# Kernel tuning notes

Measured on AMD Instinct MI355X. Metric: run time of the kernel, lower is better.

## Reference

```python
import jax, jax.numpy as jnp
import numpy as np

D_IN = 1024
D_OUT = 1024

def setup_inputs() -> dict:
    key = jax.random.key(0)
    kx, kq, kk, kv = jax.random.split(key, 4)
    x = jax.random.normal(kx, (4, 4096, D_IN), dtype=jnp.float32)
    s = 1.0 / np.sqrt(D_IN)
    Wq = jax.random.uniform(kq, (D_IN, D_OUT), dtype=jnp.float32, minval=-s, maxval=s)
    Wk = jax.random.uniform(kk, (D_IN, D_OUT), dtype=jnp.float32, minval=-s, maxval=s)
    Wv = jax.random.uniform(kv, (D_IN, D_OUT), dtype=jnp.float32, minval=-s, maxval=s)
    return {"x": x, "Wq": Wq, "Wk": Wk, "Wv": Wv}

def reference(x, Wq, Wk, Wv):
    # x: [B, S, d_in]; single-head causal attention (dropout p=0 => identity)
    B, S, _ = x.shape
    Q = jnp.einsum('bsd,de->bse', x, Wq)
    K = jnp.einsum('bsd,de->bse', x, Wk)
    V = jnp.einsum('bsd,de->bse', x, Wv)
    scale = 1.0 / jnp.sqrt(jnp.asarray(K.shape[-1], dtype=Q.dtype))
    scores = jnp.einsum('bqe,bke->bqk', Q, K) * scale  # [B, S, S]
    causal = jnp.tril(jnp.ones((S, S), dtype=bool))     # mask upper triangle (diag=1)
    scores = jnp.where(causal, scores, -jnp.inf)
    weights = jax.nn.softmax(scores, axis=-1)
    return jnp.einsum('bqk,bke->bqe', weights, V)
```

## Files before the change

### kernel.cpp

```cpp
#include <hip/hip_runtime.h>
#include <hip/hip_bf16.h>
#include <stdint.h>

typedef short short8 __attribute__((ext_vector_type(8)));
typedef short short4v __attribute__((ext_vector_type(4)));
typedef float f32x4 __attribute__((ext_vector_type(4)));

static __device__ __forceinline__ short f2bf(float f) {
  union { float f; uint32_t u; } v; v.f = f;
  uint32_t r = (v.u + 0x7fffu + ((v.u >> 16) & 1u)) >> 16;
  return (short)(uint16_t)r;
}
static __device__ __forceinline__ float bf2f(short h) {
  union { uint32_t u; float f; } v; v.u = ((uint32_t)(uint16_t)h) << 16;
  return v.f;
}

#define MFMA(a, b, c) __builtin_amdgcn_mfma_f32_16x16x32_bf16((a), (b), (c), 0, 0, 0)

static __device__ __forceinline__ void gload16(const short* g, short* l) {
  __builtin_amdgcn_global_load_lds(
      (const __attribute__((address_space(1))) void*)g,
      (__attribute__((address_space(3))) void*)l, 16, 0, 0);
}

static __device__ __forceinline__ void gemm_tile(
    const short* __restrict__ Ag, int lda,
    const short* __restrict__ Bg, int ldb, int kext,
    short* Alds, short* Blds, int w, int lane, f32x4 (&acc)[4][4])
{
  const int wr = (w >> 1) * 64, wc = (w & 1) * 64;
  const int lr = lane & 15, lk = lane >> 4;

  const int c0 = w * 128 + lane;
  const int c1 = c0 + 64;
  const int r0 = c0 >> 2, ch0 = (c0 & 3) ^ ((r0 >> 1) & 3);
  const int r1 = c1 >> 2, ch1 = (c1 & 3) ^ ((r1 >> 1) & 3);
  const short* a0 = Ag + (size_t)r0 * lda + ch0 * 8;
  const short* a1 = Ag + (size_t)r1 * lda + ch1 * 8;
  const short* b0 = Bg + (size_t)r0 * ldb + ch0 * 8;
  const short* b1 = Bg + (size_t)r1 * ldb + ch1 * 8;
  short* la0 = Alds + w * 1024;
  short* la1 = la0 + 512;
  short* lb0 = Blds + w * 1024;
  short* lb1 = lb0 + 512;

  int ra[4], rb[4];
#pragma unroll
  for (int mt = 0; mt < 4; ++mt) {
    int rl = wr + mt * 16 + lr;
    ra[mt] = rl * 32 + (lk ^ ((rl >> 1) & 3)) * 8;
  }
#pragma unroll
  for (int nt = 0; nt < 4; ++nt) {
    int rl = wc + nt * 16 + lr;
    rb[nt] = rl * 32 + (lk ^ ((rl >> 1) & 3)) * 8;
  }

  for (int kk = 0; kk < kext; kk += 32) {
    if (kk) __syncthreads();
    gload16(a0 + kk, la0);
    gload16(a1 + kk, la1);
    gload16(b0 + kk, lb0);
    gload16(b1 + kk, lb1);
    __syncthreads();
    short8 af[4], bfr[4];
#pragma unroll
    for (int mt = 0; mt < 4; ++mt) af[mt] = *(const short8*)&Alds[ra[mt]];
#pragma unroll
    for (int nt = 0; nt < 4; ++nt) bfr[nt] = *(const short8*)&Blds[rb[nt]];
#pragma unroll
    for (int mt = 0; mt < 4; ++mt)
#pragma unroll
      for (int nt = 0; nt < 4; ++nt)
        acc[mt][nt] = MFMA(af[mt], bfr[nt], acc[mt][nt]);
  }
}

__global__ __launch_bounds__(256)
void cvt_x(const float* __restrict__ x, short* __restrict__ xb) {
  size_t i = (size_t)blockIdx.x * 256 + threadIdx.x;
  f32x4 a = *(const f32x4*)(x + i * 8);
  f32x4 b = *(const f32x4*)(x + i * 8 + 4);
  short8 h = { f2bf(a.x), f2bf(a.y), f2bf(a.z), f2bf(a.w),
               f2bf(b.x), f2bf(b.y), f2bf(b.z), f2bf(b.w) };
  *(short8*)(xb + i * 8) = h;
}

__global__ __launch_bounds__(256)
void cvt_w(const float* __restrict__ Wq, const float* __restrict__ Wk,
           const float* __restrict__ Wv, short* __restrict__ wt) {
  __shared__ short Tl[128][136];
  const int z = blockIdx.z;
  const float* W = (z == 0) ? Wq : (z == 1) ? Wk : Wv;
  const float scale = (z == 0) ? 0.03125f : 1.0f;
  const int c0 = blockIdx.x * 128, r0 = blockIdx.y * 128;
  const int t = threadIdx.x;
#pragma unroll
  for (int j = 0; j < 16; ++j) {
    int id = j * 256 + t;
    int row = id >> 5, c4 = id & 31;
    f32x4 v = *(const f32x4*)(W + (size_t)(r0 + row) * 1024 + c0 + c4 * 4);
#pragma unroll
    for (int cc = 0; cc < 4; ++cc) Tl[c4 * 4 + cc][row] = f2bf(v[cc] * scale);
  }
  __syncthreads();
  short* dst = wt + (size_t)z * 1048576;
#pragma unroll
  for (int j = 0; j < 8; ++j) {
    int id = j * 256 + t;
    int col = id >> 4, r8 = id & 15;
    *(short8*)(dst + (size_t)(c0 + col) * 1024 + r0 + r8 * 8) =
        *(const short8*)&Tl[col][r8 * 8];
  }
}

__global__ __launch_bounds__(256)
void qkv_gemm(const short* __restrict__ xb, const short* __restrict__ wt,
              short* __restrict__ q, short* __restrict__ k,
              short* __restrict__ vt) {
  __shared__ short Alds[128 * 32], Blds[128 * 32];
  const int z = blockIdx.z;
  const int n0 = blockIdx.x * 128, m0 = blockIdx.y * 128;
  const int t = threadIdx.x, w = t >> 6, lane = t & 63;
  f32x4 acc[4][4] = {};
  gemm_tile(xb + (size_t)m0 * 1024, 1024,
            wt + (size_t)z * 1048576 + (size_t)n0 * 1024, 1024, 1024,
            Alds, Blds, w, lane, acc);
  const int lr = lane & 15, lk = lane >> 4;
  const int wr = (w >> 1) * 64, wc = (w & 1) * 64;
#pragma unroll
  for (int mt = 0; mt < 4; ++mt) {
#pragma unroll
    for (int nt = 0; nt < 4; ++nt) {
      int col = n0 + wc + nt * 16 + lr;
      int rbase = m0 + wr + mt * 16 + lk * 4;
      if (z == 2) {
        int b = rbase >> 12, s = rbase & 4095;
        short4v h = { f2bf(acc[mt][nt][0]), f2bf(acc[mt][nt][1]),
                      f2bf(acc[mt][nt][2]), f2bf(acc[mt][nt][3]) };
        *(short4v*)(vt + ((size_t)b * 1024 + col) * 4096 + s) = h;
      } else {
        short* dst = (z == 0) ? q : k;
#pragma unroll
        for (int i = 0; i < 4; ++i)
          dst[(size_t)(rbase + i) * 1024 + col] = f2bf(acc[mt][nt][i]);
      }
    }
  }
}

__global__ __launch_bounds__(256)
void s_gemm(const short* __restrict__ q, const short* __restrict__ k,
            short* __restrict__ P, float* __restrict__ lpart) {
  __shared__ short Alds[128 * 32], Blds[128 * 32];
  const int bid = blockIdx.x;
  const int b = bid & 3, tt = bid >> 2;
  int ti = (int)((sqrtf(8.f * tt + 1.f) - 1.f) * 0.5f);
  while ((ti + 1) * (ti + 2) / 2 <= tt) ++ti;
  while (ti * (ti + 1) / 2 > tt) --ti;
  const int tj = tt - ti * (ti + 1) / 2;
  const int t = threadIdx.x, w = t >> 6, lane = t & 63;
  f32x4 acc[4][4] = {};
  gemm_tile(q + ((size_t)(b * 4096 + ti * 128)) * 1024, 1024,
            k + ((size_t)(b * 4096 + tj * 128)) * 1024, 1024, 1024,
            Alds, Blds, w, lane, acc);
  const int lr = lane & 15, lk = lane >> 4;
  const int wr = (w >> 1) * 64, wc = (w & 1) * 64;
#pragma unroll
  for (int mt = 0; mt < 4; ++mt) {
    int rl0 = wr + mt * 16 + lk * 4;
#pragma unroll
    for (int i = 0; i < 4; ++i) {
      int rl = rl0 + i;
      size_t prow = ((size_t)(b * 4096 + ti * 128 + rl)) * 4096 + tj * 128;
      float rs = 0.f;
#pragma unroll
      for (int nt = 0; nt < 4; ++nt) {
        int cl = wc + nt * 16 + lr;
        float e = 0.f;
        if (ti != tj || cl <= rl) e = __expf(acc[mt][nt][i]);
        short pb = f2bf(e);
        P[prow + cl] = pb;
        rs += bf2f(pb);
      }
      rs += __shfl_xor(rs, 1);
      rs += __shfl_xor(rs, 2);
      rs += __shfl_xor(rs, 4);
      rs += __shfl_xor(rs, 8);
      if (lr == 0)
        lpart[((size_t)(tj * 2 + (w & 1))) * 16384 + b * 4096 + ti * 128 + rl] = rs;
    }
  }
}

__global__ __launch_bounds__(256)
void l_reduce(const float* __restrict__ lpart, float* __restrict__ lsum) {
  int idx = blockIdx.x * 256 + threadIdx.x;
  int qq = idx & 4095;
  int ti = qq >> 7;
  float s = 0.f;
  for (int tj = 0; tj <= ti; ++tj)
    s += lpart[(size_t)(tj * 2) * 16384 + idx] +
         lpart[(size_t)(tj * 2 + 1) * 16384 + idx];
  lsum[idx] = s;
}

__global__ __launch_bounds__(256)
void pv_gemm(const short* __restrict__ P, const short* __restrict__ vt,
             const float* __restrict__ lsum, float* __restrict__ out) {
  __shared__ short Alds[128 * 32], Blds[128 * 32];
  const int bid = blockIdx.x;
  const int b = bid & 3;
  const int r = bid >> 2;
  const int dt = r & 7;
  const int qt = 31 - (r >> 3);
  const int t = threadIdx.x, w = t >> 6, lane = t & 63;
  f32x4 acc[4][4] = {};
  gemm_tile(P + ((size_t)(b * 4096 + qt * 128)) * 4096, 4096,
            vt + ((size_t)(b * 1024 + dt * 128)) * 4096, 4096,
            (qt + 1) * 128, Alds, Blds, w, lane, acc);
  const int lr = lane & 15, lk = lane >> 4;
  const int wr = (w >> 1) * 64, wc = (w & 1) * 64;
#pragma unroll
  for (int mt = 0; mt < 4; ++mt) {
#pragma unroll
    for (int i = 0; i < 4; ++i) {
      int rl = wr + mt * 16 + lk * 4 + i;
      int grow = b * 4096 + qt * 128 + rl;
      float inv = 1.0f / lsum[grow];
#pragma unroll
      for (int nt = 0; nt < 4; ++nt) {
        int cl = wc + nt * 16 + lr;
        out[(size_t)grow * 1024 + dt * 128 + cl] = acc[mt][nt][i] * inv;
      }
    }
  }
}

extern "C" void kernel_launch(void* const* d_in, const int* in_sizes, int n_in,
                              void* d_out, int out_size, void* d_ws, size_t ws_size,
                              hipStream_t stream) {
  (void)in_sizes; (void)n_in; (void)out_size; (void)ws_size;
  const float* x  = (const float*)d_in[0];
  const float* Wq = (const float*)d_in[1];
  const float* Wk = (const float*)d_in[2];
  const float* Wv = (const float*)d_in[3];
  float* out = (float*)d_out;

  short* q_ws  = (short*)d_ws;
  short* k_ws  = q_ws + (size_t)16777216;
  short* vt_ws = k_ws + (size_t)16777216;
  short* P     = vt_ws + (size_t)16777216;
  short* xb    = P;
  float* lpart = (float*)(P + (size_t)67108864);
  float* lsum  = lpart + (size_t)33 * 2 * 16384;
  short* wt    = (short*)(lsum + 16384);

  cvt_x<<<dim3(8192), 256, 0, stream>>>(x, xb);
  cvt_w<<<dim3(8, 8, 3), 256, 0, stream>>>(Wq, Wk, Wv, wt);
  qkv_gemm<<<dim3(8, 128, 3), 256, 0, stream>>>(xb, wt, q_ws, k_ws, vt_ws);
  s_gemm<<<dim3(2112), 256, 0, stream>>>(q_ws, k_ws, P, lpart);
  l_reduce<<<dim3(64), 256, 0, stream>>>(lpart, lsum);
  pv_gemm<<<dim3(1024), 256, 0, stream>>>(P, vt_ws, lsum, out);
}
```

Before: 375.6 us.

## Replace GEMM tile loop with 4-stage LDS-pipelined 512-thread kernel

Rewrites the shared GEMM helper as a multi-buffered pipeline. Four 64-wide K stages sit in 128 KB of dynamic LDS, loads are issued three steps ahead, and completion is gated with explicit vmcnt waits and one barrier per step. Blocks grow to 512 threads with 8 waves, each computing a 64x32 sub-tile, and the partial row-sum layout widens to 4 slices per tile. The aim is to hide global-load latency and halve the barrier count per K step. In exchange it uses much more LDS, which may cap occupancy, and it depends on exact waitcnt accounting.

```diff
diff --git a/kernel.cpp b/kernel.cpp
--- a/kernel.cpp
+++ b/kernel.cpp
@@ -24,56 +24,86 @@
       (__attribute__((address_space(3))) void*)l, 16, 0, 0);
 }
 
-static __device__ __forceinline__ void gemm_tile(
+static __device__ __forceinline__ void stage_tile(
+    const short* __restrict__ Ag, int lda,
+    const short* __restrict__ Bg, int ldb, int kk,
+    short* slot, int t, int w)
+{
+#pragma unroll
+  for (int j = 0; j < 2; ++j) {
+    int idx = j * 512 + t;
+    int row = idx >> 3;
+    int cg = (idx & 7) ^ (row & 7);
+    gload16(Ag + (size_t)row * lda + kk + cg * 8, slot + j * 4096 + w * 512);
+  }
+#pragma unroll
+  for (int j = 0; j < 2; ++j) {
+    int idx = j * 512 + t;
+    int row = idx >> 3;
+    int cg = (idx & 7) ^ (row & 7);
+    gload16(Bg + (size_t)row * ldb + kk + cg * 8, slot + 8192 + j * 4096 + w * 512);
+  }
+}
+
+static __device__ __forceinline__ void gemm_pipe(
     const short* __restrict__ Ag, int lda,
     const short* __restrict__ Bg, int ldb, int kext,
-    short* Alds, short* Blds, int w, int lane, f32x4 (&acc)[4][4])
+    short* lds, int t, f32x4 (&acc)[4][2])
 {
-  const int wr = (w >> 1) * 64, wc = (w & 1) * 64;
+  const int w  = t >> 6, lane = t & 63;
   const int lr = lane & 15, lk = lane >> 4;
-
-  const int c0 = w * 128 + lane;
-  const int c1 = c0 + 64;
-  const int r0 = c0 >> 2, ch0 = (c0 & 3) ^ ((r0 >> 1) & 3);
-  const int r1 = c1 >> 2, ch1 = (c1 & 3) ^ ((r1 >> 1) & 3);
-  const short* a0 = Ag + (size_t)r0 * lda + ch0 * 8;
-  const short* a1 = Ag + (size_t)r1 * lda + ch1 * 8;
-  const short* b0 = Bg + (size_t)r0 * ldb + ch0 * 8;
-  const short* b1 = Bg + (size_t)r1 * ldb + ch1 * 8;
-  short* la0 = Alds + w * 1024;
-  short* la1 = la0 + 512;
-  short* lb0 = Blds + w * 1024;
-  short* lb1 = lb0 + 512;
-
-  int ra[4], rb[4];
-#pragma unroll
-  for (int mt = 0; mt < 4; ++mt) {
-    int rl = wr + mt * 16 + lr;
-    ra[mt] = rl * 32 + (lk ^ ((rl >> 1) & 3)) * 8;
-  }
-#pragma unroll
-  for (int nt = 0; nt < 4; ++nt) {
-    int rl = wc + nt * 16 + lr;
-    rb[nt] = rl * 32 + (lk ^ ((rl >> 1) & 3)) * 8;
-  }
-
-  for (int kk = 0; kk < kext; kk += 32) {
-    if (kk) __syncthreads();
-    gload16(a0 + kk, la0);
-    gload16(a1 + kk, la1);
-    gload16(b0 + kk, lb0);
-    gload16(b1 + kk, lb1);
-    __syncthreads();
-    short8 af[4], bfr[4];
-#pragma unroll
-    for (int mt = 0; mt < 4; ++mt) af[mt] = *(const short8*)&Alds[ra[mt]];
-#pragma unroll
-    for (int nt = 0; nt < 4; ++nt) bfr[nt] = *(const short8*)&Blds[rb[nt]];
-#pragma unroll
-    for (int mt = 0; mt < 4; ++mt)
-#pragma unroll
-      for (int nt = 0; nt < 4; ++nt)
-        acc[mt][nt] = MFMA(af[mt], bfr[nt], acc[mt][nt]);
+  const int wr64 = (w >> 2) * 64, wc32 = (w & 3) * 32;
+  const int nk = kext >> 6;
+
+  const int npro = nk < 3 ? nk : 3;
+  for (int p = 0; p < npro; ++p)
+    stage_tile(Ag, lda, Bg, ldb, p * 64, lds + p * 16384, t, w);
+
+  for (int tt = 0; tt < nk; ++tt) {
+    const int rem = nk - 1 - tt;
+    if (rem >= 2)      { asm volatile("s_waitcnt vmcnt(8)" ::: "memory"); }
+    else if (rem == 1) { asm volatile("s_waitcnt vmcnt(4)" ::: "memory"); }
+    else               { asm volatile("s_waitcnt vmcnt(0)" ::: "memory"); }
+    __builtin_amdgcn_sched_barrier(0);
+    __builtin_amdgcn_s_barrier();
+    __builtin_amdgcn_sched_barrier(0);
+
+    if (tt + 3 < nk)
+      stage_tile(Ag, lda, Bg, ldb, (tt + 3) * 64,
+                 lds + ((tt + 3) & 3) * 16384, t, w);
+
+    short* slot = lds + (tt & 3) * 16384;
+    short8 af[4][2], bfr[2][2];
+#pragma unroll
+    for (int mt = 0; mt < 4; ++mt) {
+      int rl = wr64 + mt * 16 + lr;
+#pragma unroll
+      for (int kh = 0; kh < 2; ++kh) {
+        int ch = (kh * 4 + lk) ^ (rl & 7);
+        af[mt][kh] = *(const short8*)&slot[rl * 64 + ch * 8];
+      }
+    }
+#pragma unroll
+    for (int nt = 0; nt < 2; ++nt) {
+      int rl = wc32 + nt * 16 + lr;
+#pragma unroll
+      for (int kh = 0; kh < 2; ++kh) {
+        int ch = (kh * 4 + lk) ^ (rl & 7);
+        bfr[nt][kh] = *(const short8*)&slot[8192 + rl * 64 + ch * 8];
+      }
+    }
+    __builtin_amdgcn_s_setprio(1);
+#pragma unroll
+    for (int kh = 0; kh < 2; ++kh)
+#pragma unroll
+      for (int mt = 0; mt < 4; ++mt)
+#pragma unroll
+        for (int nt = 0; nt < 2; ++nt)
+          acc[mt][nt] = MFMA(af[mt][kh], bfr[nt][kh], acc[mt][nt]);
+    __builtin_amdgcn_s_setprio(0);
+
+    asm volatile("s_waitcnt lgkmcnt(0)" ::: "memory");
+    __builtin_amdgcn_sched_barrier(0);
   }
 }
 
@@ -115,26 +145,27 @@
   }
 }
 
-__global__ __launch_bounds__(256)
+__global__ __launch_bounds__(512, 2)
 void qkv_gemm(const short* __restrict__ xb, const short* __restrict__ wt,
               short* __restrict__ q, short* __restrict__ k,
               short* __restrict__ vt) {
-  __shared__ short Alds[128 * 32], Blds[128 * 32];
+  extern __shared__ short lds[];
   const int z = blockIdx.z;
   const int n0 = blockIdx.x * 128, m0 = blockIdx.y * 128;
-  const int t = threadIdx.x, w = t >> 6, lane = t & 63;
-  f32x4 acc[4][4] = {};
-  gemm_tile(xb + (size_t)m0 * 1024, 1024,
+  const int t = threadIdx.x;
+  f32x4 acc[4][2] = {};
+  gemm_pipe(xb + (size_t)m0 * 1024, 1024,
             wt + (size_t)z * 1048576 + (size_t)n0 * 1024, 1024, 1024,
-            Alds, Blds, w, lane, acc);
+            lds, t, acc);
+  const int w = t >> 6, lane = t & 63;
   const int lr = lane & 15, lk = lane >> 4;
-  const int wr = (w >> 1) * 64, wc = (w & 1) * 64;
+  const int wr64 = (w >> 2) * 64, wc32 = (w & 3) * 32;
 #pragma unroll
   for (int mt = 0; mt < 4; ++mt) {
 #pragma unroll
-    for (int nt = 0; nt < 4; ++nt) {
-      int col = n0 + wc + nt * 16 + lr;
-      int rbase = m0 + wr + mt * 16 + lk * 4;
+    for (int nt = 0; nt < 2; ++nt) {
+      int col = n0 + wc32 + nt * 16 + lr;
+      int rbase = m0 + wr64 + mt * 16 + lk * 4;
       if (z == 2) {
         int b = rbase >> 12, s = rbase & 4095;
         short4v h = { f2bf(acc[mt][nt][0]), f2bf(acc[mt][nt][1]),
@@ -150,34 +181,35 @@
   }
 }
 
-__global__ __launch_bounds__(256)
+__global__ __launch_bounds__(512, 2)
 void s_gemm(const short* __restrict__ q, const short* __restrict__ k,
             short* __restrict__ P, float* __restrict__ lpart) {
-  __shared__ short Alds[128 * 32], Blds[128 * 32];
+  extern __shared__ short lds[];
   const int bid = blockIdx.x;
   const int b = bid & 3, tt = bid >> 2;
   int ti = (int)((sqrtf(8.f * tt + 1.f) - 1.f) * 0.5f);
   while ((ti + 1) * (ti + 2) / 2 <= tt) ++ti;
   while (ti * (ti + 1) / 2 > tt) --ti;
   const int tj = tt - ti * (ti + 1) / 2;
-  const int t = threadIdx.x, w = t >> 6, lane = t & 63;
-  f32x4 acc[4][4] = {};
-  gemm_tile(q + ((size_t)(b * 4096 + ti * 128)) * 1024, 1024,
+  const int t = threadIdx.x;
+  f32x4 acc[4][2] = {};
+  gemm_pipe(q + ((size_t)(b * 4096 + ti * 128)) * 1024, 1024,
             k + ((size_t)(b * 4096 + tj * 128)) * 1024, 1024, 1024,
-            Alds, Blds, w, lane, acc);
+            lds, t, acc);
+  const int w = t >> 6, lane = t & 63;
   const int lr = lane & 15, lk = lane >> 4;
-  const int wr = (w >> 1) * 64, wc = (w & 1) * 64;
+  const int wr64 = (w >> 2) * 64, wc32 = (w & 3) * 32;
 #pragma unroll
   for (int mt = 0; mt < 4; ++mt) {
-    int rl0 = wr + mt * 16 + lk * 4;
+    int rl0 = wr64 + mt * 16 + lk * 4;
 #pragma unroll
     for (int i = 0; i < 4; ++i) {
       int rl = rl0 + i;
       size_t prow = ((size_t)(b * 4096 + ti * 128 + rl)) * 4096 + tj * 128;
       float rs = 0.f;
 #pragma unroll
-      for (int nt = 0; nt < 4; ++nt) {
-        int cl = wc + nt * 16 + lr;
+      for (int nt = 0; nt < 2; ++nt) {
+        int cl = wc32 + nt * 16 + lr;
         float e = 0.f;
         if (ti != tj || cl <= rl) e = __expf(acc[mt][nt][i]);
         short pb = f2bf(e);
@@ -189,7 +221,7 @@
       rs += __shfl_xor(rs, 4);
       rs += __shfl_xor(rs, 8);
       if (lr == 0)
-        lpart[((size_t)(tj * 2 + (w & 1))) * 16384 + b * 4096 + ti * 128 + rl] = rs;
+        lpart[((size_t)(tj * 4 + (w & 3))) * 16384 + b * 4096 + ti * 128 + rl] = rs;
     }
   }
 }
@@ -200,38 +232,42 @@
   int qq = idx & 4095;
   int ti = qq >> 7;
   float s = 0.f;
-  for (int tj = 0; tj <= ti; ++tj)
-    s += lpart[(size_t)(tj * 2) * 16384 + idx] +
-         lpart[(size_t)(tj * 2 + 1) * 16384 + idx];
+  for (int tj = 0; tj <= ti; ++tj) {
+    s += lpart[(size_t)(tj * 4 + 0) * 16384 + idx] +
+         lpart[(size_t)(tj * 4 + 1) * 16384 + idx] +
+         lpart[(size_t)(tj * 4 + 2) * 16384 + idx] +
+         lpart[(size_t)(tj * 4 + 3) * 16384 + idx];
+  }
   lsum[idx] = s;
 }
 
-__global__ __launch_bounds__(256)
+__global__ __launch_bounds__(512, 2)
 void pv_gemm(const short* __restrict__ P, const short* __restrict__ vt,
              const float* __restrict__ lsum, float* __restrict__ out) {
-  __shared__ short Alds[128 * 32], Blds[128 * 32];
+  extern __shared__ short lds[];
   const int bid = blockIdx.x;
   const int b = bid & 3;
   const int r = bid >> 2;
   const int dt = r & 7;
   const int qt = 31 - (r >> 3);
-  const int t = threadIdx.x, w = t >> 6, lane = t & 63;
-  f32x4 acc[4][4] = {};
-  gemm_tile(P + ((size_t)(b * 4096 + qt * 128)) * 4096, 4096,
+  const int t = threadIdx.x;
+  f32x4 acc[4][2] = {};
+  gemm_pipe(P + ((size_t)(b * 4096 + qt * 128)) * 4096, 4096,
             vt + ((size_t)(b * 1024 + dt * 128)) * 4096, 4096,
-            (qt + 1) * 128, Alds, Blds, w, lane, acc);
+            (qt + 1) * 128, lds, t, acc);
+  const int w = t >> 6, lane = t & 63;
   const int lr = lane & 15, lk = lane >> 4;
-  const int wr = (w >> 1) * 64, wc = (w & 1) * 64;
+  const int wr64 = (w >> 2) * 64, wc32 = (w & 3) * 32;
 #pragma unroll
   for (int mt = 0; mt < 4; ++mt) {
 #pragma unroll
     for (int i = 0; i < 4; ++i) {
-      int rl = wr + mt * 16 + lk * 4 + i;
+      int rl = wr64 + mt * 16 + lk * 4 + i;
       int grow = b * 4096 + qt * 128 + rl;
       float inv = 1.0f / lsum[grow];
 #pragma unroll
-      for (int nt = 0; nt < 4; ++nt) {
-        int cl = wc + nt * 16 + lr;
+      for (int nt = 0; nt < 2; ++nt) {
+        int cl = wc32 + nt * 16 + lr;
         out[(size_t)grow * 1024 + dt * 128 + cl] = acc[mt][nt][i] * inv;
       }
     }
@@ -254,13 +290,21 @@
   short* P     = vt_ws + (size_t)16777216;
   short* xb    = P;
   float* lpart = (float*)(P + (size_t)67108864);
-  float* lsum  = lpart + (size_t)33 * 2 * 16384;
+  float* lsum  = lpart + (size_t)128 * 16384;
   short* wt    = (short*)(lsum + 16384);
+
+  const int gemm_lds = 4 * 16384 * 2;
+  hipFuncSetAttribute((const void*)qkv_gemm,
+                      hipFuncAttributeMaxDynamicSharedMemorySize, gemm_lds);
+  hipFuncSetAttribute((const void*)s_gemm,
+                      hipFuncAttributeMaxDynamicSharedMemorySize, gemm_lds);
+  hipFuncSetAttribute((const void*)pv_gemm,
+                      hipFuncAttributeMaxDynamicSharedMemorySize, gemm_lds);
 
   cvt_x<<<dim3(8192), 256, 0, stream>>>(x, xb);
   cvt_w<<<dim3(8, 8, 3), 256, 0, stream>>>(Wq, Wk, Wv, wt);
-  qkv_gemm<<<dim3(8, 128, 3), 256, 0, stream>>>(xb, wt, q_ws, k_ws, vt_ws);
-  s_gemm<<<dim3(2112), 256, 0, stream>>>(q_ws, k_ws, P, lpart);
+  qkv_gemm<<<dim3(8, 128, 3), 512, gemm_lds, stream>>>(xb, wt, q_ws, k_ws, vt_ws);
+  s_gemm<<<dim3(2112), 512, gemm_lds, stream>>>(q_ws, k_ws, P, lpart);
   l_reduce<<<dim3(64), 256, 0, stream>>>(lpart, lsum);
-  pv_gemm<<<dim3(1024), 256, 0, stream>>>(P, vt_ws, lsum, out);
-}
+  pv_gemm<<<dim3(1024), 512, gemm_lds, stream>>>(P, vt_ws, lsum, out);
+}
```

Result: slower. 393.7 us (+4.8%).

## Use 256x256 double-buffered pipelined GEMM tiles for QKV and score kernels

Applied to the files above, without the earlier changes.

Adds a new GEMM core that computes 256x256 output tiles with 512 threads. It uses a K-step of 64, double-buffered LDS (128KB dynamic) with XOR swizzle, and interleaves global-to-LDS prefetch of the next stage with MFMA on the current one, raising MFMA priority with setprio. The QKV projection and the causal score kernel switch to this core, and the triangular tile indexing, row-sum partials and l_reduce are adjusted for the 256 tile size. The aim is more data reuse per loaded byte and hiding of load latency. In exchange it costs more registers and LDS per block, and diagonal tiles become coarser, so more masked work is computed.

```diff
diff --git a/kernel.cpp b/kernel.cpp
--- a/kernel.cpp
+++ b/kernel.cpp
@@ -24,7 +24,90 @@
       (__attribute__((address_space(3))) void*)l, 16, 0, 0);
 }
 
-static __device__ __forceinline__ void gemm_tile(
+static __device__ __forceinline__ void gemm256_pipe(
+    const short* __restrict__ Ag, int lda,
+    const short* __restrict__ Bg, int ldb, int kext,
+    short* lds, int t, f32x4 (&acc)[8][4])
+{
+  const int w = t >> 6, lane = t & 63;
+  const int lr = lane & 15, lk = lane >> 4;
+  const int wm = w >> 2, wn = w & 3;
+  const int nk = kext >> 6;
+
+  const int sr0 = t >> 3;          const int sc0 = (t & 7) ^ (sr0 & 7);
+  const int sr1 = (512 + t) >> 3;  const int sc1 = (t & 7) ^ (sr1 & 7);
+  const int ch0 = (lk ^ (lr & 7)) * 8;
+  const int ch1 = ((4 + lk) ^ (lr & 7)) * 8;
+
+#pragma unroll
+  for (int h = 0; h < 2; ++h) {
+    gload16(Ag + (size_t)(h * 128 + sr0) * lda + sc0 * 8, lds + h * 8192 + w * 512);
+    gload16(Ag + (size_t)(h * 128 + sr1) * lda + sc1 * 8, lds + h * 8192 + 4096 + w * 512);
+    gload16(Bg + (size_t)(h * 128 + sr0) * ldb + sc0 * 8, lds + 32768 + h * 8192 + w * 512);
+    gload16(Bg + (size_t)(h * 128 + sr1) * ldb + sc1 * 8, lds + 32768 + h * 8192 + 4096 + w * 512);
+  }
+  asm volatile("s_waitcnt vmcnt(0)" ::: "memory");
+  __builtin_amdgcn_s_barrier();
+
+  for (int g = 0; g < nk; ++g) {
+    short* Ac = lds + ((g & 1) << 14);
+    short* Bc = lds + 32768 + ((g & 1) << 14);
+    short* An = lds + (((g + 1) & 1) << 14);
+    short* Bn = lds + 32768 + (((g + 1) & 1) << 14);
+    const int kk = (g + 1) << 6;
+    const bool st = (g + 1 < nk);
+
+    short8 bfr[4][2];
+#pragma unroll
+    for (int q = 0; q < 4; ++q) {
+      short8 af[2][2];
+#pragma unroll
+      for (int mtl = 0; mtl < 2; ++mtl) {
+        const int rbase = (wm * 128 + (2 * q + mtl) * 16 + lr) * 64;
+        af[mtl][0] = *(const short8*)&Ac[rbase + ch0];
+        af[mtl][1] = *(const short8*)&Ac[rbase + ch1];
+      }
+      if (q == 0) {
+#pragma unroll
+        for (int nt = 0; nt < 4; ++nt) {
+          const int rbase = (wn * 64 + nt * 16 + lr) * 64;
+          bfr[nt][0] = *(const short8*)&Bc[rbase + ch0];
+          bfr[nt][1] = *(const short8*)&Bc[rbase + ch1];
+        }
+      }
+      if (st && q == 0) {
+#pragma unroll
+        for (int h = 0; h < 2; ++h) {
+          gload16(Ag + (size_t)(h * 128 + sr0) * lda + kk + sc0 * 8, An + h * 8192 + w * 512);
+          gload16(Ag + (size_t)(h * 128 + sr1) * lda + kk + sc1 * 8, An + h * 8192 + 4096 + w * 512);
+        }
+      }
+      if (st && q == 1) {
+#pragma unroll
+        for (int h = 0; h < 2; ++h) {
+          gload16(Bg + (size_t)(h * 128 + sr0) * ldb + kk + sc0 * 8, Bn + h * 8192 + w * 512);
+          gload16(Bg + (size_t)(h * 128 + sr1) * ldb + kk + sc1 * 8, Bn + h * 8192 + 4096 + w * 512);
+        }
+      }
+      __builtin_amdgcn_s_barrier();
+      asm volatile("s_waitcnt lgkmcnt(0)" ::: "memory");
+      __builtin_amdgcn_sched_barrier(0);
+      __builtin_amdgcn_s_setprio(1);
+#pragma unroll
+      for (int kh = 0; kh < 2; ++kh)
+#pragma unroll
+        for (int mtl = 0; mtl < 2; ++mtl)
+#pragma unroll
+          for (int nt = 0; nt < 4; ++nt)
+            acc[2 * q + mtl][nt] = MFMA(af[mtl][kh], bfr[nt][kh], acc[2 * q + mtl][nt]);
+      __builtin_amdgcn_s_setprio(0);
+      if (q == 3) asm volatile("s_waitcnt vmcnt(0)" ::: "memory");
+      __builtin_amdgcn_s_barrier();
+    }
+  }
+}
+
+static __device__ __forceinline__ void gemm_tile128(
     const short* __restrict__ Ag, int lda,
     const short* __restrict__ Bg, int ldb, int kext,
     short* Alds, short* Blds, int w, int lane, f32x4 (&acc)[4][4])
@@ -34,12 +117,12 @@
 
   const int c0 = w * 128 + lane;
   const int c1 = c0 + 64;
-  const int r0 = c0 >> 2, ch0 = (c0 & 3) ^ ((r0 >> 1) & 3);
-  const int r1 = c1 >> 2, ch1 = (c1 & 3) ^ ((r1 >> 1) & 3);
-  const short* a0 = Ag + (size_t)r0 * lda + ch0 * 8;
-  const short* a1 = Ag + (size_t)r1 * lda + ch1 * 8;
-  const short* b0 = Bg + (size_t)r0 * ldb + ch0 * 8;
-  const short* b1 = Bg + (size_t)r1 * ldb + ch1 * 8;
+  const int r0 = c0 >> 2, cg0 = (c0 & 3) ^ ((r0 >> 1) & 3);
+  const int r1 = c1 >> 2, cg1 = (c1 & 3) ^ ((r1 >> 1) & 3);
+  const short* a0 = Ag + (size_t)r0 * lda + cg0 * 8;
+  const short* a1 = Ag + (size_t)r1 * lda + cg1 * 8;
+  const short* b0 = Bg + (size_t)r0 * ldb + cg0 * 8;
+  const short* b1 = Bg + (size_t)r1 * ldb + cg1 * 8;
   short* la0 = Alds + w * 1024;
   short* la1 = la0 + 512;
   short* lb0 = Blds + w * 1024;
@@ -115,31 +198,32 @@
   }
 }
 
-__global__ __launch_bounds__(256)
+__global__ __launch_bounds__(512, 2)
 void qkv_gemm(const short* __restrict__ xb, const short* __restrict__ wt,
               short* __restrict__ q, short* __restrict__ k,
               short* __restrict__ vt) {
-  __shared__ short Alds[128 * 32], Blds[128 * 32];
+  extern __shared__ short lds[];
   const int z = blockIdx.z;
-  const int n0 = blockIdx.x * 128, m0 = blockIdx.y * 128;
-  const int t = threadIdx.x, w = t >> 6, lane = t & 63;
-  f32x4 acc[4][4] = {};
-  gemm_tile(xb + (size_t)m0 * 1024, 1024,
-            wt + (size_t)z * 1048576 + (size_t)n0 * 1024, 1024, 1024,
-            Alds, Blds, w, lane, acc);
-  const int lr = lane & 15, lk = lane >> 4;
-  const int wr = (w >> 1) * 64, wc = (w & 1) * 64;
-#pragma unroll
-  for (int mt = 0; mt < 4; ++mt) {
+  const int n0 = blockIdx.x * 256, m0 = blockIdx.y * 256;
+  const int t = threadIdx.x;
+  f32x4 acc[8][4] = {};
+  gemm256_pipe(xb + (size_t)m0 * 1024, 1024,
+               wt + (size_t)z * 1048576 + (size_t)n0 * 1024, 1024, 1024,
+               lds, t, acc);
+  const int w = t >> 6, lane = t & 63;
+  const int lr = lane & 15, lk = lane >> 4;
+  const int wm = w >> 2, wn = w & 3;
+#pragma unroll
+  for (int mt = 0; mt < 8; ++mt) {
 #pragma unroll
     for (int nt = 0; nt < 4; ++nt) {
-      int col = n0 + wc + nt * 16 + lr;
-      int rbase = m0 + wr + mt * 16 + lk * 4;
+      int col = n0 + wn * 64 + nt * 16 + lr;
+      int rbase = m0 + wm * 128 + mt * 16 + lk * 4;
       if (z == 2) {
-        int b = rbase >> 12, s = rbase & 4095;
+        int bb = rbase >> 12, s = rbase & 4095;
         short4v h = { f2bf(acc[mt][nt][0]), f2bf(acc[mt][nt][1]),
                       f2bf(acc[mt][nt][2]), f2bf(acc[mt][nt][3]) };
-        *(short4v*)(vt + ((size_t)b * 1024 + col) * 4096 + s) = h;
+        *(short4v*)(vt + ((size_t)bb * 1024 + col) * 4096 + s) = h;
       } else {
         short* dst = (z == 0) ? q : k;
 #pragma unroll
@@ -150,36 +234,36 @@
   }
 }
 
-__global__ __launch_bounds__(256)
+__global__ __launch_bounds__(512, 2)
 void s_gemm(const short* __restrict__ q, const short* __restrict__ k,
             short* __restrict__ P, float* __restrict__ lpart) {
-  __shared__ short Alds[128 * 32], Blds[128 * 32];
+  extern __shared__ short lds[];
   const int bid = blockIdx.x;
   const int b = bid & 3, tt = bid >> 2;
   int ti = (int)((sqrtf(8.f * tt + 1.f) - 1.f) * 0.5f);
   while ((ti + 1) * (ti + 2) / 2 <= tt) ++ti;
   while (ti * (ti + 1) / 2 > tt) --ti;
   const int tj = tt - ti * (ti + 1) / 2;
-  const int t = threadIdx.x, w = t >> 6, lane = t & 63;
-  f32x4 acc[4][4] = {};
-  gemm_tile(q + ((size_t)(b * 4096 + ti * 128)) * 1024, 1024,
-            k + ((size_t)(b * 4096 + tj * 128)) * 1024, 1024, 1024,
-            Alds, Blds, w, lane, acc);
-  const int lr = lane & 15, lk = lane >> 4;
-  const int wr = (w >> 1) * 64, wc = (w & 1) * 64;
-#pragma unroll
-  for (int mt = 0; mt < 4; ++mt) {
-    int rl0 = wr + mt * 16 + lk * 4;
+  const int t = threadIdx.x;
+  f32x4 acc[8][4] = {};
+  gemm256_pipe(q + ((size_t)(b * 4096 + ti * 256)) * 1024, 1024,
+               k + ((size_t)(b * 4096 + tj * 256)) * 1024, 1024, 1024,
+               lds, t, acc);
+  const int w = t >> 6, lane = t & 63;
+  const int lr = lane & 15, lk = lane >> 4;
+  const int wm = w >> 2, wn = w & 3;
+  const bool diag = (ti == tj);
+#pragma unroll
+  for (int mt = 0; mt < 8; ++mt) {
 #pragma unroll
     for (int i = 0; i < 4; ++i) {
-      int rl = rl0 + i;
-      size_t prow = ((size_t)(b * 4096 + ti * 128 + rl)) * 4096 + tj * 128;
+      const int rl = wm * 128 + mt * 16 + lk * 4 + i;
+      size_t prow = ((size_t)(b * 4096 + ti * 256 + rl)) * 4096 + tj * 256;
       float rs = 0.f;
 #pragma unroll
       for (int nt = 0; nt < 4; ++nt) {
-        int cl = wc + nt * 16 + lr;
-        float e = 0.f;
-        if (ti != tj || cl <= rl) e = __expf(acc[mt][nt][i]);
+        const int cl = wn * 64 + nt * 16 + lr;
+        float e = (!diag || cl <= rl) ? __expf(acc[mt][nt][i]) : 0.f;
         short pb = f2bf(e);
         P[prow + cl] = pb;
         rs += bf2f(pb);
@@ -189,7 +273,7 @@
       rs += __shfl_xor(rs, 4);
       rs += __shfl_xor(rs, 8);
       if (lr == 0)
-        lpart[((size_t)(tj * 2 + (w & 1))) * 16384 + b * 4096 + ti * 128 + rl] = rs;
+        lpart[((size_t)(tj * 4 + wn)) * 16384 + b * 4096 + ti * 256 + rl] = rs;
     }
   }
 }
@@ -198,11 +282,13 @@
 void l_reduce(const float* __restrict__ lpart, float* __restrict__ lsum) {
   int idx = blockIdx.x * 256 + threadIdx.x;
   int qq = idx & 4095;
-  int ti = qq >> 7;
+  int ti = qq >> 8;
   float s = 0.f;
-  for (int tj = 0; tj <= ti; ++tj)
-    s += lpart[(size_t)(tj * 2) * 16384 + idx] +
-         lpart[(size_t)(tj * 2 + 1) * 16384 + idx];
+  for (int tj = 0; tj <= ti; ++tj) {
+#pragma unroll
+    for (int e = 0; e < 4; ++e)
+      s += lpart[(size_t)(tj * 4 + e) * 16384 + idx];
+  }
   lsum[idx] = s;
 }
 
@@ -217,9 +303,9 @@
   const int qt = 31 - (r >> 3);
   const int t = threadIdx.x, w = t >> 6, lane = t & 63;
   f32x4 acc[4][4] = {};
-  gemm_tile(P + ((size_t)(b * 4096 + qt * 128)) * 4096, 4096,
-            vt + ((size_t)(b * 1024 + dt * 128)) * 4096, 4096,
-            (qt + 1) * 128, Alds, Blds, w, lane, acc);
+  gemm_tile128(P + ((size_t)(b * 4096 + qt * 128)) * 4096, 4096,
+               vt + ((size_t)(b * 1024 + dt * 128)) * 4096, 4096,
+               (qt + 1) * 128, Alds, Blds, w, lane, acc);
   const int lr = lane & 15, lk = lane >> 4;
   const int wr = (w >> 1) * 64, wc = (w & 1) * 64;
 #pragma unroll
@@ -254,13 +340,19 @@
   short* P     = vt_ws + (size_t)16777216;
   short* xb    = P;
   float* lpart = (float*)(P + (size_t)67108864);
-  float* lsum  = lpart + (size_t)33 * 2 * 16384;
+  float* lsum  = lpart + (size_t)64 * 16384;
   short* wt    = (short*)(lsum + 16384);
+
+  const int gemm_lds = 131072;
+  hipFuncSetAttribute((const void*)qkv_gemm,
+                      hipFuncAttributeMaxDynamicSharedMemorySize, gemm_lds);
+  hipFuncSetAttribute((const void*)s_gemm,
+                      hipFuncAttributeMaxDynamicSharedMemorySize, gemm_lds);
 
   cvt_x<<<dim3(8192), 256, 0, stream>>>(x, xb);
   cvt_w<<<dim3(8, 8, 3), 256, 0, stream>>>(Wq, Wk, Wv, wt);
-  qkv_gemm<<<dim3(8, 128, 3), 256, 0, stream>>>(xb, wt, q_ws, k_ws, vt_ws);
-  s_gemm<<<dim3(2112), 256, 0, stream>>>(q_ws, k_ws, P, lpart);
+  qkv_gemm<<<dim3(4, 64, 3), 512, gemm_lds, stream>>>(xb, wt, q_ws, k_ws, vt_ws);
+  s_gemm<<<dim3(544), 512, gemm_lds, stream>>>(q_ws, k_ws, P, lpart);
   l_reduce<<<dim3(64), 256, 0, stream>>>(lpart, lsum);
   pv_gemm<<<dim3(1024), 256, 0, stream>>>(P, vt_ws, lsum, out);
 }
```

Result: faster. 340.2 us (-9.4%).
